# Kernel tuning notes

Measured on AMD Instinct MI355X. Metric: run time of the kernel, lower is better.

Reference implementation:

```python
import jax, jax.numpy as jnp
import numpy as np

B, S, D, H = 2, 2048, 1024, 16
DK = D // H


def setup_inputs() -> dict:
    key = jax.random.key(0)
    ks = jax.random.split(key, 12)
    s = 1.0 / np.sqrt(D)
    return {
        "query": jax.random.normal(ks[0], (B, S, D), dtype=jnp.float32),
        "key": jax.random.normal(ks[1], (B, S, D), dtype=jnp.float32),
        "value": jax.random.normal(ks[2], (B, S, D), dtype=jnp.float32),
        "mask": jax.random.randint(ks[3], (B, 1, 1, S), 0, 2, dtype=jnp.int32),
        "wq": jax.random.normal(ks[4], (D, D), dtype=jnp.float32) * s,
        "bq": jnp.zeros((D,), dtype=jnp.float32),
        "wk": jax.random.normal(ks[5], (D, D), dtype=jnp.float32) * s,
        "bk": jnp.zeros((D,), dtype=jnp.float32),
        "wv": jax.random.normal(ks[6], (D, D), dtype=jnp.float32) * s,
        "bv": jnp.zeros((D,), dtype=jnp.float32),
        "wo": jax.random.normal(ks[7], (D, D), dtype=jnp.float32) * s,
        "bo": jnp.zeros((D,), dtype=jnp.float32),
    }


def reference(query, key, value, mask, wq, bq, wk, bk, wv, bv, wo, bo):
    b, s, d = query.shape
    # torch Linear: y = x @ W^T + b, then split heads -> [B, H, S, dk]
    def proj(x, w, bias):
        return (x @ w.T + bias).reshape(b, -1, H, DK).transpose(0, 2, 1, 3)

    q = proj(query, wq, bq)
    k = proj(key, wk, bk)
    v = proj(value, wv, bv)

    scores = jnp.einsum("bhqd,bhkd->bhqk", q, k) / jnp.sqrt(jnp.float32(DK))
    scores = jnp.where(mask == 0, jnp.float32(-1e9), scores)
    attn = jax.nn.softmax(scores, axis=-1)  # [B,H,S,S]
    x = jnp.einsum("bhqk,bhkd->bhqd", attn, v)
    x = x.transpose(0, 2, 1, 3).reshape(b, s, d)
    return x @ wo.T + bo
```

## Files before the change

### kernel.cpp

```cpp
#include <hip/hip_runtime.h>
#include <math.h>

#define B_  2
#define S_  2048
#define D_  1024
#define H_  16
#define DK_ 64

typedef unsigned short u16;
typedef unsigned int u32;
typedef __bf16 bf16x8 __attribute__((ext_vector_type(8)));
typedef float f32x4 __attribute__((ext_vector_type(4)));
typedef float f32x16 __attribute__((ext_vector_type(16)));
typedef u32 u32x2 __attribute__((ext_vector_type(2)));
typedef u32 u32x4 __attribute__((ext_vector_type(4)));

typedef const __attribute__((address_space(1))) void* gas1_t;
typedef __attribute__((address_space(3))) void* las3_t;

__device__ __forceinline__ void gload_lds16(const void* g, void* l) {
    __builtin_amdgcn_global_load_lds((gas1_t)g, (las3_t)l, 16, 0, 0);
}

__device__ __forceinline__ u16 f2bf(float f) {
    union { float f; unsigned u; } v; v.f = f;
    return (u16)((v.u + 0x7fffu + ((v.u >> 16) & 1u)) >> 16);
}

__device__ __forceinline__ u32 pack_bf16_2(float lo, float hi) {
    union { float f; u32 u; } a, b;
    a.f = lo; b.f = hi;
    return __builtin_amdgcn_perm(b.u + 0x8000u, a.u + 0x8000u, 0x07060302u);
}

__device__ __forceinline__ u32 cvtpk_bf16(float lo, float hi) {
    u32 r;
    asm("v_cvt_pk_bf16_f32 %0, %1, %2" : "=v"(r) : "v"(lo), "v"(hi));
    return r;
}

__global__ __launch_bounds__(256)
void cast_all(const float* __restrict__ q, const float* __restrict__ k,
              const float* __restrict__ v, const float* __restrict__ wq,
              const float* __restrict__ wk, const float* __restrict__ wv,
              const float* __restrict__ wo, const int* __restrict__ mask,
              u16* __restrict__ qb, u16* __restrict__ kb, u16* __restrict__ vb,
              u16* __restrict__ wqb, u16* __restrict__ wkb, u16* __restrict__ wvb,
              u16* __restrict__ wob, float* __restrict__ mfac,
              float* __restrict__ nmaskf)
{
    const int bi = blockIdx.x;
    const int tid = threadIdx.x;
    if (bi >= 2064) {
        const int b = bi - 2064;
        __shared__ int red[256];
        int c = 0;
#pragma unroll
        for (int j = 0; j < 8; ++j)
            c += (mask[b * S_ + tid * 8 + j] == 0) ? 1 : 0;
        red[tid] = c;
        __syncthreads();
        for (int s = 128; s > 0; s >>= 1) {
            if (tid < s) red[tid] += red[tid + s];
            __syncthreads();
        }
        if (tid == 0) nmaskf[b] = (float)red[0];
        return;
    }
    if (bi >= 2048) {
        const int idx = (bi - 2048) * 256 + tid;
        mfac[idx] = mask[idx] ? 1.0f : 0.0f;
        return;
    }
#pragma unroll
    for (int j = 0; j < 8; ++j) {
        const int i = bi * 256 + tid + j * 524288;
        const float* src; u16* dst; int off;
        if (i < 3 * 1048576) {
            const int seg = i >> 20; off = i & 1048575;
            src = (seg == 0) ? q : (seg == 1) ? k : v;
            dst = (seg == 0) ? qb : (seg == 1) ? kb : vb;
        } else {
            const int jj = i - 3 * 1048576;
            const int seg = jj >> 18; off = jj & 262143;
            src = (seg == 0) ? wq : (seg == 1) ? wk : (seg == 2) ? wv : wo;
            dst = (seg == 0) ? wqb : (seg == 1) ? wkb : (seg == 2) ? wvb : wob;
        }
        const float4 val = ((const float4*)src)[off];
        uint2 o;
        o.x = pack_bf16_2(val.x, val.y);
        o.y = pack_bf16_2(val.z, val.w);
        ((uint2*)dst)[off] = o;
    }
}

template<int BM, int BN>
__device__ __forceinline__ void gemm_body(
    const u16* __restrict__ A, const u16* __restrict__ W,
    const float* __restrict__ bias, void* __restrict__ outp,
    float scale, int mode, int m0, int n0,
    const float* __restrict__ rowfac, const float* __restrict__ colfac)
{
    constexpr int MI = BM / 32;
    constexpr int NJ = BN / 32;
    __shared__ u16 sA[BM * 64];
    __shared__ u16 sW[BN * 64];

    const int tid  = threadIdx.x;
    const int wave = tid >> 6, lane = tid & 63;
    const int quad = lane >> 4, l16 = lane & 15;
    const int wm = (wave >> 1) * (BM / 2);
    const int wn = (wave & 1) * (BN / 2);
    const int srow = lane >> 3;
    const int scol = ((lane & 7) ^ srow) * 8;
    const int sw7  = l16 & 7;

    f32x4 acc[MI][NJ];
    const f32x4 zero = {0.f, 0.f, 0.f, 0.f};
#pragma unroll
    for (int i = 0; i < MI; ++i)
#pragma unroll
        for (int j = 0; j < NJ; ++j) acc[i][j] = zero;

    const u16* ast = A + (size_t)(m0 + wave * 8 + srow) * D_ + scol;
    const u16* wst = W + (size_t)(n0 + wave * 8 + srow) * D_ + scol;

    for (int k0 = 0; k0 < D_; k0 += 64) {
#pragma unroll
        for (int t = 0; t < BM / 32; ++t)
            gload_lds16(ast + (size_t)t * 32 * D_ + k0, sA + (wave + t * 4) * 512);
#pragma unroll
        for (int t = 0; t < BN / 32; ++t)
            gload_lds16(wst + (size_t)t * 32 * D_ + k0, sW + (wave + t * 4) * 512);
        __syncthreads();

#pragma unroll
        for (int kh = 0; kh < 2; ++kh) {
            const int phys = ((kh * 4 + quad) ^ sw7) * 8;
            bf16x8 af[MI], bfr[NJ];
#pragma unroll
            for (int i = 0; i < MI; ++i)
                af[i] = *(const bf16x8*)(sA + (wm + i * 16 + l16) * 64 + phys);
#pragma unroll
            for (int j = 0; j < NJ; ++j)
                bfr[j] = *(const bf16x8*)(sW + (wn + j * 16 + l16) * 64 + phys);
#pragma unroll
            for (int i = 0; i < MI; ++i)
#pragma unroll
                for (int j = 0; j < NJ; ++j)
                    acc[i][j] = __builtin_amdgcn_mfma_f32_16x16x32_bf16(af[i], bfr[j], acc[i][j], 0, 0, 0);
        }
        __syncthreads();
    }

#pragma unroll
    for (int i = 0; i < MI; ++i) {
        float rf4[4];
        if (mode == 1 && rowfac) {
#pragma unroll
            for (int r = 0; r < 4; ++r)
                rf4[r] = rowfac[m0 + wm + i * 16 + quad * 4 + r];
        }
#pragma unroll
        for (int j = 0; j < NJ; ++j) {
            const int n = n0 + wn + j * 16 + l16;
            if (mode == 3) {
                const float cf = colfac ? colfac[n] : 1.0f;
#pragma unroll
                for (int r = 0; r < 4; ++r) {
                    const int mp = m0 + wm + i * 16 + quad * 4 + r;
                    ((u16*)outp)[(size_t)mp * (B_ * S_) + n] = f2bf((acc[i][j][r] + bias[mp]) * cf);
                }
            } else {
                const float bn = bias[n];
#pragma unroll
                for (int r = 0; r < 4; ++r) {
                    const int m = m0 + wm + i * 16 + quad * 4 + r;
                    float v = acc[i][j][r] + bn;
                    if (mode == 0) {
                        ((float*)outp)[(size_t)m * D_ + n] = v;
                    } else {
                        v *= scale;
                        if (rowfac) v *= rf4[r];
                        const int b = m >> 11, s = m & (S_ - 1);
                        const int h = n >> 6, dk = n & 63;
                        ((u16*)outp)[(((size_t)(b * H_ + h)) * S_ + s) * DK_ + dk] = f2bf(v);
                    }
                }
            }
        }
    }
}

__global__ __launch_bounds__(256)
void qkv_gemm(const u16* __restrict__ qin, const u16* __restrict__ kin, const u16* __restrict__ vin,
              const u16* __restrict__ wqb, const u16* __restrict__ wkb, const u16* __restrict__ wvb,
              const float* __restrict__ bq, const float* __restrict__ bk, const float* __restrict__ bv,
              u16* __restrict__ Qp, u16* __restrict__ Kp, u16* __restrict__ Vt,
              const float* __restrict__ mfac)
{
    const int bid = blockIdx.x;
    const int swz = (bid & 7) * 192 + (bid >> 3);
    const int z   = swz >> 9;
    const int rem = swz & 511;

    if (z == 2) {
        const int mi = rem & 15, ni = rem >> 4;
        gemm_body<64, 128>(wvb, vin, bv, Vt, 1.0f, 3, mi * 64, ni * 128,
                           nullptr, mfac);
    } else {
        const int by = rem >> 3;
        const int bx = rem & 7;
        const u16* A = (z == 0) ? qin : kin;
        const u16* W = (z == 0) ? wqb : wkb;
        const float* bias = (z == 0) ? bq : bk;
        u16* outp = (z == 0) ? Qp : Kp;
        const float scale = (z == 0) ? 0.18033688011112042f : 1.0f;
        const float* rf = (z == 1) ? mfac : nullptr;
        gemm_body<64, 128>(A, W, bias, outp, scale, 1, by * 64, bx * 128,
                           rf, nullptr);
    }
}

__global__ __launch_bounds__(256)
void out_gemm(const u16* __restrict__ Xc, const u16* __restrict__ wob,
              const float* __restrict__ bo, float* __restrict__ out)
{
    const int bid = blockIdx.x;
    const int swz = (bid & 7) * 128 + (bid >> 3);
    const int by  = swz >> 4;
    const int bx  = swz & 15;
    gemm_body<64, 64>(Xc, wob, bo, out, 1.0f, 0, by * 64, bx * 64,
                      nullptr, nullptr);
}

__global__ __launch_bounds__(512, 4)
void attn_mfma(const u16* __restrict__ Qp, const u16* __restrict__ Kp,
               const u16* __restrict__ Vt, const float* __restrict__ nmaskf,
               u16* __restrict__ Xc)
{
    __shared__ u16 sKV[2][2][8192];

    const int tid  = threadIdx.x;
    const int wave = tid >> 6, lane = tid & 63;
    const int qg = wave & 3, kg = wave >> 2;
    const int l31 = lane & 31, hi = lane >> 5;
    const int bid = blockIdx.x;
    const int swz = (bid & 7) * 64 + (bid >> 3);
    const int qt = swz & 15;
    const int bh = swz >> 4;
    const int b  = bh >> 4;
    const int h  = bh & 15;
    const int lr  = lane >> 3;
    const int cl  = (lane & 7) ^ lr;
    const int sw5 = l31 & 7;

    const u16* Qb = Qp + ((size_t)bh * S_ + qt * 128) * DK_;
    const u16* Kb = Kp + (size_t)bh * S_ * DK_;
    const int vdk = (qg * 8 + lr) + 32 * (cl >> 2);
    const u16* Vsrc = Vt + (size_t)(h * 64 + vdk) * (B_ * S_) + b * S_ + (cl & 3) * 8;
    const u16* Ksrc = Kb + (size_t)(qg * 8 + lr) * DK_ + cl * 8;

    bf16x8 qf[4];
    {
        const u16* qrow = Qb + (size_t)(qg * 32 + l31) * DK_ + hi * 8;
        qf[0] = *(const bf16x8*)(qrow);
        qf[1] = *(const bf16x8*)(qrow + 16);
        qf[2] = *(const bf16x8*)(qrow + 32);
        qf[3] = *(const bf16x8*)(qrow + 48);
    }

    const u16* kpre = Ksrc + (size_t)kg * 64 * DK_;
    const u16* vpre = Vsrc + kg * 64;
    {
        u16* dst = sKV[kg][0];
        gload_lds16(kpre,                    dst + qg * 512);
        gload_lds16(kpre + (size_t)32 * DK_, dst + 2048 + qg * 512);
        gload_lds16(vpre,                    dst + 4096 + qg * 512);
        gload_lds16(vpre + 32,               dst + 6144 + qg * 512);
        kpre += (size_t)128 * DK_;
        vpre += 128;
    }

    f32x16 oc[2];
    const f32x16 z16 = {0.f,0.f,0.f,0.f,0.f,0.f,0.f,0.f,
                        0.f,0.f,0.f,0.f,0.f,0.f,0.f,0.f};
    oc[0] = z16; oc[1] = z16;
    float lsum = 0.f;

    for (int i = 0; i < 16; ++i) {
        __syncthreads();
        const int cur = i & 1;

        if (i < 15) {
            u16* dst = sKV[kg][cur ^ 1];
            gload_lds16(kpre,                    dst + qg * 512);
            gload_lds16(kpre + (size_t)32 * DK_, dst + 2048 + qg * 512);
            gload_lds16(vpre,                    dst + 4096 + qg * 512);
            gload_lds16(vpre + 32,               dst + 6144 + qg * 512);
            kpre += (size_t)128 * DK_;
            vpre += 128;
        }
        const u16* sKA = sKV[kg][cur];
        const u16* sKB = sKA + 2048;
        const u16* sVA = sKA + 4096;
        const u16* sVB = sKA + 6144;

        f32x16 sfrA, sfrB;
        {
            const bf16x8 a0 = *(const bf16x8*)(sKA + l31 * 64 + (((0 + hi) ^ sw5)) * 8);
            const bf16x8 a1 = *(const bf16x8*)(sKA + l31 * 64 + (((2 + hi) ^ sw5)) * 8);
            const bf16x8 a2 = *(const bf16x8*)(sKA + l31 * 64 + (((4 + hi) ^ sw5)) * 8);
            const bf16x8 a3 = *(const bf16x8*)(sKA + l31 * 64 + (((6 + hi) ^ sw5)) * 8);
            const bf16x8 b0 = *(const bf16x8*)(sKB + l31 * 64 + (((0 + hi) ^ sw5)) * 8);
            const bf16x8 b1 = *(const bf16x8*)(sKB + l31 * 64 + (((2 + hi) ^ sw5)) * 8);
            const bf16x8 b2 = *(const bf16x8*)(sKB + l31 * 64 + (((4 + hi) ^ sw5)) * 8);
            const bf16x8 b3 = *(const bf16x8*)(sKB + l31 * 64 + (((6 + hi) ^ sw5)) * 8);
            __builtin_amdgcn_s_setprio(1);
            sfrA = __builtin_amdgcn_mfma_f32_32x32x16_bf16(a0, qf[0], z16, 0, 0, 0);
            sfrB = __builtin_amdgcn_mfma_f32_32x32x16_bf16(b0, qf[0], z16, 0, 0, 0);
            sfrA = __builtin_amdgcn_mfma_f32_32x32x16_bf16(a1, qf[1], sfrA, 0, 0, 0);
            sfrB = __builtin_amdgcn_mfma_f32_32x32x16_bf16(b1, qf[1], sfrB, 0, 0, 0);
            sfrA = __builtin_amdgcn_mfma_f32_32x32x16_bf16(a2, qf[2], sfrA, 0, 0, 0);
            sfrB = __builtin_amdgcn_mfma_f32_32x32x16_bf16(b2, qf[2], sfrB, 0, 0, 0);
            sfrA = __builtin_amdgcn_mfma_f32_32x32x16_bf16(a3, qf[3], sfrA, 0, 0, 0);
            sfrB = __builtin_amdgcn_mfma_f32_32x32x16_bf16(b3, qf[3], sfrB, 0, 0, 0);
            __builtin_amdgcn_s_setprio(0);
        }

        {
            float p[16];
#pragma unroll
            for (int r = 0; r < 16; ++r) p[r] = __builtin_amdgcn_exp2f(sfrA[r]);
            const float s0 = (p[0] + p[1]) + (p[2] + p[3]);
            const float s1 = (p[4] + p[5]) + (p[6] + p[7]);
            const float s2 = (p[8] + p[9]) + (p[10] + p[11]);
            const float s3 = (p[12] + p[13]) + (p[14] + p[15]);
            lsum += (s0 + s1) + (s2 + s3);
            const u32 W00 = cvtpk_bf16(p[0], p[1]);
            const u32 W01 = cvtpk_bf16(p[2], p[3]);
            const u32 W10 = cvtpk_bf16(p[4], p[5]);
            const u32 W11 = cvtpk_bf16(p[6], p[7]);
            const u32 W20 = cvtpk_bf16(p[8], p[9]);
            const u32 W21 = cvtpk_bf16(p[10], p[11]);
            const u32 W30 = cvtpk_bf16(p[12], p[13]);
            const u32 W31 = cvtpk_bf16(p[14], p[15]);
            const u32x2 e0 = __builtin_amdgcn_permlane32_swap(W00, W10, false, false);
            const u32x2 e1 = __builtin_amdgcn_permlane32_swap(W01, W11, false, false);
            const u32x2 e2 = __builtin_amdgcn_permlane32_swap(W20, W30, false, false);
            const u32x2 e3 = __builtin_amdgcn_permlane32_swap(W21, W31, false, false);
            u32x4 A0 = { e0[0], e1[0], e0[1], e1[1] };
            u32x4 A1 = { e2[0], e3[0], e2[1], e3[1] };
            const bf16x8 pa0 = *(const bf16x8*)&A0;
            const bf16x8 pa1 = *(const bf16x8*)&A1;
            const bf16x8 v00 = *(const bf16x8*)(sVA + l31 * 64 + (((0 + hi) ^ sw5)) * 8);
            const bf16x8 v01 = *(const bf16x8*)(sVA + l31 * 64 + (((2 + hi) ^ sw5)) * 8);
            const bf16x8 v10 = *(const bf16x8*)(sVA + l31 * 64 + (((4 + hi) ^ sw5)) * 8);
            const bf16x8 v11 = *(const bf16x8*)(sVA + l31 * 64 + (((6 + hi) ^ sw5)) * 8);
            __builtin_amdgcn_s_setprio(1);
            oc[0] = __builtin_amdgcn_mfma_f32_32x32x16_bf16(pa0, v00, oc[0], 0, 0, 0);
            oc[1] = __builtin_amdgcn_mfma_f32_32x32x16_bf16(pa0, v10, oc[1], 0, 0, 0);
            oc[0] = __builtin_amdgcn_mfma_f32_32x32x16_bf16(pa1, v01, oc[0], 0, 0, 0);
            oc[1] = __builtin_amdgcn_mfma_f32_32x32x16_bf16(pa1, v11, oc[1], 0, 0, 0);
            __builtin_amdgcn_s_setprio(0);
        }

        {
            float p[16];
#pragma unroll
            for (int r = 0; r < 16; ++r) p[r] = __builtin_amdgcn_exp2f(sfrB[r]);
            const float s0 = (p[0] + p[1]) + (p[2] + p[3]);
            const float s1 = (p[4] + p[5]) + (p[6] + p[7]);
            const float s2 = (p[8] + p[9]) + (p[10] + p[11]);
            const float s3 = (p[12] + p[13]) + (p[14] + p[15]);
            lsum += (s0 + s1) + (s2 + s3);
            const u32 W00 = cvtpk_bf16(p[0], p[1]);
            const u32 W01 = cvtpk_bf16(p[2], p[3]);
            const u32 W10 = cvtpk_bf16(p[4], p[5]);
            const u32 W11 = cvtpk_bf16(p[6], p[7]);
            const u32 W20 = cvtpk_bf16(p[8], p[9]);
            const u32 W21 = cvtpk_bf16(p[10], p[11]);
            const u32 W30 = cvtpk_bf16(p[12], p[13]);
            const u32 W31 = cvtpk_bf16(p[14], p[15]);
            const u32x2 e0 = __builtin_amdgcn_permlane32_swap(W00, W10, false, false);
            const u32x2 e1 = __builtin_amdgcn_permlane32_swap(W01, W11, false, false);
            const u32x2 e2 = __builtin_amdgcn_permlane32_swap(W20, W30, false, false);
            const u32x2 e3 = __builtin_amdgcn_permlane32_swap(W21, W31, false, false);
            u32x4 A0 = { e0[0], e1[0], e0[1], e1[1] };
            u32x4 A1 = { e2[0], e3[0], e2[1], e3[1] };
            const bf16x8 pa0 = *(const bf16x8*)&A0;
            const bf16x8 pa1 = *(const bf16x8*)&A1;
            const bf16x8 v00 = *(const bf16x8*)(sVB + l31 * 64 + (((0 + hi) ^ sw5)) * 8);
            const bf16x8 v01 = *(const bf16x8*)(sVB + l31 * 64 + (((2 + hi) ^ sw5)) * 8);
            const bf16x8 v10 = *(const bf16x8*)(sVB + l31 * 64 + (((4 + hi) ^ sw5)) * 8);
            const bf16x8 v11 = *(const bf16x8*)(sVB + l31 * 64 + (((6 + hi) ^ sw5)) * 8);
            __builtin_amdgcn_s_setprio(1);
            oc[0] = __builtin_amdgcn_mfma_f32_32x32x16_bf16(pa0, v00, oc[0], 0, 0, 0);
            oc[1] = __builtin_amdgcn_mfma_f32_32x32x16_bf16(pa0, v10, oc[1], 0, 0, 0);
            oc[0] = __builtin_amdgcn_mfma_f32_32x32x16_bf16(pa1, v01, oc[0], 0, 0, 0);
            oc[1] = __builtin_amdgcn_mfma_f32_32x32x16_bf16(pa1, v11, oc[1], 0, 0, 0);
            __builtin_amdgcn_s_setprio(0);
        }
    }

    {
        union { float f; u32 u; } lu; lu.f = lsum;
        const u32x2 lr2 = __builtin_amdgcn_permlane32_swap(lu.u, lu.u, false, false);
        union { u32 u; float f; } pu; pu.u = hi ? lr2[0] : lr2[1];
        lsum += pu.f;
    }

    __syncthreads();
    float* sO = (float*)&sKV[0][0][0];
    float* sL = (float*)((char*)sO + 32768);
    if (hi == 0) sL[kg * 128 + qg * 32 + l31] = lsum;
    if (kg == 1) {
#pragma unroll
        for (int dh = 0; dh < 2; ++dh)
#pragma unroll
            for (int g = 0; g < 4; ++g) {
                f32x4 t = { oc[dh][g * 4 + 0], oc[dh][g * 4 + 1],
                            oc[dh][g * 4 + 2], oc[dh][g * 4 + 3] };
                *(f32x4*)(sO + qg * 2048 + ((dh * 4 + g) * 2 + hi) * 128 + l31 * 4) = t;
            }
    }
    __syncthreads();
    if (kg == 0) {
        const float nm = nmaskf[b];
#pragma unroll
        for (int g = 0; g < 4; ++g) {
            const f32x4 oA = *(const f32x4*)(sO + qg * 2048 + ((0 + g) * 2 + hi) * 128 + l31 * 4);
            const f32x4 oB = *(const f32x4*)(sO + qg * 2048 + ((4 + g) * 2 + hi) * 128 + l31 * 4);
#pragma unroll
            for (int rr = 0; rr < 4; ++rr) {
                const int qrow = rr + 8 * g + 4 * hi;
                const float inv = __builtin_amdgcn_rcpf(
                    sL[qg * 32 + qrow] + sL[128 + qg * 32 + qrow] - nm);
                const int s = qt * 128 + qg * 32 + qrow;
                const size_t base = ((size_t)(b * S_ + s)) * D_ + h * 64 + l31;
                Xc[base]      = f2bf((oc[0][g * 4 + rr] + oA[rr]) * inv);
                Xc[base + 32] = f2bf((oc[1][g * 4 + rr] + oB[rr]) * inv);
            }
        }
    }
}

extern "C" void kernel_launch(void* const* d_in, const int* in_sizes, int n_in,
                              void* d_out, int out_size, void* d_ws, size_t ws_size,
                              hipStream_t stream)
{
    (void)in_sizes; (void)n_in; (void)out_size; (void)ws_size;

    const float* query = (const float*)d_in[0];
    const float* key   = (const float*)d_in[1];
    const float* value = (const float*)d_in[2];
    const int*   mask  = (const int*)d_in[3];
    const float* wq    = (const float*)d_in[4];
    const float* bq    = (const float*)d_in[5];
    const float* wk    = (const float*)d_in[6];
    const float* bk    = (const float*)d_in[7];
    const float* wv    = (const float*)d_in[8];
    const float* bv    = (const float*)d_in[9];
    const float* wo    = (const float*)d_in[10];
    const float* bo    = (const float*)d_in[11];

    const size_t NE = (size_t)B_ * S_ * D_;
    const size_t WE = (size_t)D_ * D_;

    u16* qb  = (u16*)d_ws;
    u16* kb  = qb + NE;
    u16* vb  = kb + NE;
    u16* wqb = vb + NE;
    u16* wkb = wqb + WE;
    u16* wvb = wkb + WE;
    u16* wob = wvb + WE;
    u16* Qp  = wob + WE;
    u16* Kp  = Qp + NE;
    u16* Vt  = Kp + NE;
    float* mfac   = (float*)(Vt + NE);
    float* nmaskf = mfac + 4096;
    u16* Xc  = qb;

    cast_all<<<2066, 256, 0, stream>>>(query, key, value, wq, wk, wv, wo, mask,
                                       qb, kb, vb, wqb, wkb, wvb, wob, mfac, nmaskf);

    qkv_gemm<<<1536, 256, 0, stream>>>(
        qb, kb, vb, wqb, wkb, wvb, bq, bk, bv, Qp, Kp, Vt, mfac);

    attn_mfma<<<512, 512, 0, stream>>>(Qp, Kp, Vt, nmaskf, Xc);

    out_gemm<<<1024, 256, 0, stream>>>(Xc, wob, bo, (float*)d_out);
}
```

Baseline: 211.1 us.

## Split attention block into 64-query tiles with four-way key split

The attention kernel now gives each block 64 query rows instead of 128, and its 8 waves are arranged as 2 query groups by 4 key groups instead of 4 by 2. Each wave handles one 32-key slab per iteration instead of two, and the grid doubles to 1024 blocks. The final reduction merges three partial outputs and four row sums through shared memory. The aim is more blocks in flight and shorter per-wave dependency chains, at the cost of reloading K/V per query tile, a heavier cross-wave reduction, and less independent MFMA work per wave to hide latency.

```diff
diff --git a/kernel.cpp b/kernel.cpp
--- a/kernel.cpp
+++ b/kernel.cpp
@@ -239,23 +239,23 @@
                const u16* __restrict__ Vt, const float* __restrict__ nmaskf,
                u16* __restrict__ Xc)
 {
-    __shared__ u16 sKV[2][2][8192];
+    __shared__ u16 sKV[4][2][4096];
 
     const int tid  = threadIdx.x;
     const int wave = tid >> 6, lane = tid & 63;
-    const int qg = wave & 3, kg = wave >> 2;
+    const int qg = wave & 1, kg = wave >> 1;
     const int l31 = lane & 31, hi = lane >> 5;
     const int bid = blockIdx.x;
-    const int swz = (bid & 7) * 64 + (bid >> 3);
-    const int qt = swz & 15;
-    const int bh = swz >> 4;
+    const int swz = (bid & 7) * 128 + (bid >> 3);
+    const int qt = swz & 31;
+    const int bh = swz >> 5;
     const int b  = bh >> 4;
     const int h  = bh & 15;
     const int lr  = lane >> 3;
     const int cl  = (lane & 7) ^ lr;
     const int sw5 = l31 & 7;
 
-    const u16* Qb = Qp + ((size_t)bh * S_ + qt * 128) * DK_;
+    const u16* Qb = Qp + ((size_t)bh * S_ + qt * 64) * DK_;
     const u16* Kb = Kp + (size_t)bh * S_ * DK_;
     const int vdk = (qg * 8 + lr) + 32 * (cl >> 2);
     const u16* Vsrc = Vt + (size_t)(h * 64 + vdk) * (B_ * S_) + b * S_ + (cl & 3) * 8;
@@ -270,14 +270,14 @@
         qf[3] = *(const bf16x8*)(qrow + 48);
     }
 
-    const u16* kpre = Ksrc + (size_t)kg * 64 * DK_;
-    const u16* vpre = Vsrc + kg * 64;
+    const u16* kpre = Ksrc + (size_t)kg * 32 * DK_;
+    const u16* vpre = Vsrc + kg * 32;
     {
-        u16* dst = sKV[kg][0];
-        gload_lds16(kpre,                    dst + qg * 512);
-        gload_lds16(kpre + (size_t)32 * DK_, dst + 2048 + qg * 512);
-        gload_lds16(vpre,                    dst + 4096 + qg * 512);
-        gload_lds16(vpre + 32,               dst + 6144 + qg * 512);
+        u16* dst = &sKV[kg][0][0];
+        gload_lds16(kpre,                            dst + qg * 512);
+        gload_lds16(kpre + (size_t)16 * DK_,         dst + (qg + 2) * 512);
+        gload_lds16(vpre,                            dst + 2048 + qg * 512);
+        gload_lds16(vpre + (size_t)16 * (B_ * S_),   dst + 2048 + (qg + 2) * 512);
         kpre += (size_t)128 * DK_;
         vpre += 128;
     }
@@ -293,70 +293,63 @@
         const int cur = i & 1;
 
         if (i < 15) {
-            u16* dst = sKV[kg][cur ^ 1];
-            gload_lds16(kpre,                    dst + qg * 512);
-            gload_lds16(kpre + (size_t)32 * DK_, dst + 2048 + qg * 512);
-            gload_lds16(vpre,                    dst + 4096 + qg * 512);
-            gload_lds16(vpre + 32,               dst + 6144 + qg * 512);
+            u16* dst = &sKV[kg][cur ^ 1][0];
+            gload_lds16(kpre,                            dst + qg * 512);
+            gload_lds16(kpre + (size_t)16 * DK_,         dst + (qg + 2) * 512);
+            gload_lds16(vpre,                            dst + 2048 + qg * 512);
+            gload_lds16(vpre + (size_t)16 * (B_ * S_),   dst + 2048 + (qg + 2) * 512);
             kpre += (size_t)128 * DK_;
             vpre += 128;
         }
-        const u16* sKA = sKV[kg][cur];
-        const u16* sKB = sKA + 2048;
-        const u16* sVA = sKA + 4096;
-        const u16* sVB = sKA + 6144;
-
-        f32x16 sfrA, sfrB;
+        const u16* sK = &sKV[kg][cur][0];
+        const u16* sV = sK + 2048;
+
+        f32x16 sfr;
         {
-            const bf16x8 a0 = *(const bf16x8*)(sKA + l31 * 64 + (((0 + hi) ^ sw5)) * 8);
-            const bf16x8 a1 = *(const bf16x8*)(sKA + l31 * 64 + (((2 + hi) ^ sw5)) * 8);
-            const bf16x8 a2 = *(const bf16x8*)(sKA + l31 * 64 + (((4 + hi) ^ sw5)) * 8);
-            const bf16x8 a3 = *(const bf16x8*)(sKA + l31 * 64 + (((6 + hi) ^ sw5)) * 8);
-            const bf16x8 b0 = *(const bf16x8*)(sKB + l31 * 64 + (((0 + hi) ^ sw5)) * 8);
-            const bf16x8 b1 = *(const bf16x8*)(sKB + l31 * 64 + (((2 + hi) ^ sw5)) * 8);
-            const bf16x8 b2 = *(const bf16x8*)(sKB + l31 * 64 + (((4 + hi) ^ sw5)) * 8);
-            const bf16x8 b3 = *(const bf16x8*)(sKB + l31 * 64 + (((6 + hi) ^ sw5)) * 8);
+            const bf16x8 k0 = *(const bf16x8*)(sK + l31 * 64 + (((0 + hi) ^ sw5)) * 8);
+            const bf16x8 k1 = *(const bf16x8*)(sK + l31 * 64 + (((2 + hi) ^ sw5)) * 8);
+            const bf16x8 k2 = *(const bf16x8*)(sK + l31 * 64 + (((4 + hi) ^ sw5)) * 8);
+            const bf16x8 k3 = *(const bf16x8*)(sK + l31 * 64 + (((6 + hi) ^ sw5)) * 8);
             __builtin_amdgcn_s_setprio(1);
-            sfrA = __builtin_amdgcn_mfma_f32_32x32x16_bf16(a0, qf[0], z16, 0, 0, 0);
-            sfrB = __builtin_amdgcn_mfma_f32_32x32x16_bf16(b0, qf[0], z16, 0, 0, 0);
-            sfrA = __builtin_amdgcn_mfma_f32_32x32x16_bf16(a1, qf[1], sfrA, 0, 0, 0);
-            sfrB = __builtin_amdgcn_mfma_f32_32x32x16_bf16(b1, qf[1], sfrB, 0, 0, 0);
-            sfrA = __builtin_amdgcn_mfma_f32_32x32x16_bf16(a2, qf[2], sfrA, 0, 0, 0);
-            sfrB = __builtin_amdgcn_mfma_f32_32x32x16_bf16(b2, qf[2], sfrB, 0, 0, 0);
-            sfrA = __builtin_amdgcn_mfma_f32_32x32x16_bf16(a3, qf[3], sfrA, 0, 0, 0);
-            sfrB = __builtin_amdgcn_mfma_f32_32x32x16_bf16(b3, qf[3], sfrB, 0, 0, 0);
+            sfr = __builtin_amdgcn_mfma_f32_32x32x16_bf16(k0, qf[0], z16, 0, 0, 0);
+            sfr = __builtin_amdgcn_mfma_f32_32x32x16_bf16(k1, qf[1], sfr, 0, 0, 0);
+            sfr = __builtin_amdgcn_mfma_f32_32x32x16_bf16(k2, qf[2], sfr, 0, 0, 0);
+            sfr = __builtin_amdgcn_mfma_f32_32x32x16_bf16(k3, qf[3], sfr, 0, 0, 0);
             __builtin_amdgcn_s_setprio(0);
         }
 
+        float p[16];
+#pragma unroll
+        for (int r = 0; r < 16; ++r) p[r] = __builtin_amdgcn_exp2f(sfr[r]);
         {
-            float p[16];
-#pragma unroll
-            for (int r = 0; r < 16; ++r) p[r] = __builtin_amdgcn_exp2f(sfrA[r]);
             const float s0 = (p[0] + p[1]) + (p[2] + p[3]);
             const float s1 = (p[4] + p[5]) + (p[6] + p[7]);
             const float s2 = (p[8] + p[9]) + (p[10] + p[11]);
             const float s3 = (p[12] + p[13]) + (p[14] + p[15]);
             lsum += (s0 + s1) + (s2 + s3);
-            const u32 W00 = cvtpk_bf16(p[0], p[1]);
-            const u32 W01 = cvtpk_bf16(p[2], p[3]);
-            const u32 W10 = cvtpk_bf16(p[4], p[5]);
-            const u32 W11 = cvtpk_bf16(p[6], p[7]);
-            const u32 W20 = cvtpk_bf16(p[8], p[9]);
-            const u32 W21 = cvtpk_bf16(p[10], p[11]);
-            const u32 W30 = cvtpk_bf16(p[12], p[13]);
-            const u32 W31 = cvtpk_bf16(p[14], p[15]);
-            const u32x2 e0 = __builtin_amdgcn_permlane32_swap(W00, W10, false, false);
-            const u32x2 e1 = __builtin_amdgcn_permlane32_swap(W01, W11, false, false);
-            const u32x2 e2 = __builtin_amdgcn_permlane32_swap(W20, W30, false, false);
-            const u32x2 e3 = __builtin_amdgcn_permlane32_swap(W21, W31, false, false);
-            u32x4 A0 = { e0[0], e1[0], e0[1], e1[1] };
-            u32x4 A1 = { e2[0], e3[0], e2[1], e3[1] };
-            const bf16x8 pa0 = *(const bf16x8*)&A0;
-            const bf16x8 pa1 = *(const bf16x8*)&A1;
-            const bf16x8 v00 = *(const bf16x8*)(sVA + l31 * 64 + (((0 + hi) ^ sw5)) * 8);
-            const bf16x8 v01 = *(const bf16x8*)(sVA + l31 * 64 + (((2 + hi) ^ sw5)) * 8);
-            const bf16x8 v10 = *(const bf16x8*)(sVA + l31 * 64 + (((4 + hi) ^ sw5)) * 8);
-            const bf16x8 v11 = *(const bf16x8*)(sVA + l31 * 64 + (((6 + hi) ^ sw5)) * 8);
+        }
+        const u32 W00 = cvtpk_bf16(p[0], p[1]);
+        const u32 W01 = cvtpk_bf16(p[2], p[3]);
+        const u32 W10 = cvtpk_bf16(p[4], p[5]);
+        const u32 W11 = cvtpk_bf16(p[6], p[7]);
+        const u32 W20 = cvtpk_bf16(p[8], p[9]);
+        const u32 W21 = cvtpk_bf16(p[10], p[11]);
+        const u32 W30 = cvtpk_bf16(p[12], p[13]);
+        const u32 W31 = cvtpk_bf16(p[14], p[15]);
+        const u32x2 e0 = __builtin_amdgcn_permlane32_swap(W00, W10, false, false);
+        const u32x2 e1 = __builtin_amdgcn_permlane32_swap(W01, W11, false, false);
+        const u32x2 e2 = __builtin_amdgcn_permlane32_swap(W20, W30, false, false);
+        const u32x2 e3 = __builtin_amdgcn_permlane32_swap(W21, W31, false, false);
+        u32x4 A0 = { e0[0], e1[0], e0[1], e1[1] };
+        u32x4 A1 = { e2[0], e3[0], e2[1], e3[1] };
+        const bf16x8 pa0 = *(const bf16x8*)&A0;
+        const bf16x8 pa1 = *(const bf16x8*)&A1;
+
+        {
+            const bf16x8 v00 = *(const bf16x8*)(sV + l31 * 64 + (((0 + hi) ^ sw5)) * 8);
+            const bf16x8 v01 = *(const bf16x8*)(sV + l31 * 64 + (((2 + hi) ^ sw5)) * 8);
+            const bf16x8 v10 = *(const bf16x8*)(sV + l31 * 64 + (((4 + hi) ^ sw5)) * 8);
+            const bf16x8 v11 = *(const bf16x8*)(sV + l31 * 64 + (((6 + hi) ^ sw5)) * 8);
             __builtin_amdgcn_s_setprio(1);
             oc[0] = __builtin_amdgcn_mfma_f32_32x32x16_bf16(pa0, v00, oc[0], 0, 0, 0);
             oc[1] = __builtin_amdgcn_mfma_f32_32x32x16_bf16(pa0, v10, oc[1], 0, 0, 0);
@@ -364,43 +357,6 @@
             oc[1] = __builtin_amdgcn_mfma_f32_32x32x16_bf16(pa1, v11, oc[1], 0, 0, 0);
             __builtin_amdgcn_s_setprio(0);
         }
-
-        {
-            float p[16];
-#pragma unroll
-            for (int r = 0; r < 16; ++r) p[r] = __builtin_amdgcn_exp2f(sfrB[r]);
-            const float s0 = (p[0] + p[1]) + (p[2] + p[3]);
-            const float s1 = (p[4] + p[5]) + (p[6] + p[7]);
-            const float s2 = (p[8] + p[9]) + (p[10] + p[11]);
-            const float s3 = (p[12] + p[13]) + (p[14] + p[15]);
-            lsum += (s0 + s1) + (s2 + s3);
-            const u32 W00 = cvtpk_bf16(p[0], p[1]);
-            const u32 W01 = cvtpk_bf16(p[2], p[3]);
-            const u32 W10 = cvtpk_bf16(p[4], p[5]);
-            const u32 W11 = cvtpk_bf16(p[6], p[7]);
-            const u32 W20 = cvtpk_bf16(p[8], p[9]);
-            const u32 W21 = cvtpk_bf16(p[10], p[11]);
-            const u32 W30 = cvtpk_bf16(p[12], p[13]);
-            const u32 W31 = cvtpk_bf16(p[14], p[15]);
-            const u32x2 e0 = __builtin_amdgcn_permlane32_swap(W00, W10, false, false);
-            const u32x2 e1 = __builtin_amdgcn_permlane32_swap(W01, W11, false, false);
-            const u32x2 e2 = __builtin_amdgcn_permlane32_swap(W20, W30, false, false);
-            const u32x2 e3 = __builtin_amdgcn_permlane32_swap(W21, W31, false, false);
-            u32x4 A0 = { e0[0], e1[0], e0[1], e1[1] };
-            u32x4 A1 = { e2[0], e3[0], e2[1], e3[1] };
-            const bf16x8 pa0 = *(const bf16x8*)&A0;
-            const bf16x8 pa1 = *(const bf16x8*)&A1;
-            const bf16x8 v00 = *(const bf16x8*)(sVB + l31 * 64 + (((0 + hi) ^ sw5)) * 8);
-            const bf16x8 v01 = *(const bf16x8*)(sVB + l31 * 64 + (((2 + hi) ^ sw5)) * 8);
-            const bf16x8 v10 = *(const bf16x8*)(sVB + l31 * 64 + (((4 + hi) ^ sw5)) * 8);
-            const bf16x8 v11 = *(const bf16x8*)(sVB + l31 * 64 + (((6 + hi) ^ sw5)) * 8);
-            __builtin_amdgcn_s_setprio(1);
-            oc[0] = __builtin_amdgcn_mfma_f32_32x32x16_bf16(pa0, v00, oc[0], 0, 0, 0);
-            oc[1] = __builtin_amdgcn_mfma_f32_32x32x16_bf16(pa0, v10, oc[1], 0, 0, 0);
-            oc[0] = __builtin_amdgcn_mfma_f32_32x32x16_bf16(pa1, v01, oc[0], 0, 0, 0);
-            oc[1] = __builtin_amdgcn_mfma_f32_32x32x16_bf16(pa1, v11, oc[1], 0, 0, 0);
-            __builtin_amdgcn_s_setprio(0);
-        }
     }
 
     {
@@ -412,16 +368,17 @@
 
     __syncthreads();
     float* sO = (float*)&sKV[0][0][0];
-    float* sL = (float*)((char*)sO + 32768);
-    if (hi == 0) sL[kg * 128 + qg * 32 + l31] = lsum;
-    if (kg == 1) {
+    float* sL = (float*)((char*)&sKV[0][0][0] + 49152);
+    if (hi == 0) sL[kg * 64 + qg * 32 + l31] = lsum;
+    if (kg != 0) {
+        const int slot = (kg - 1) * 2 + qg;
 #pragma unroll
         for (int dh = 0; dh < 2; ++dh)
 #pragma unroll
             for (int g = 0; g < 4; ++g) {
                 f32x4 t = { oc[dh][g * 4 + 0], oc[dh][g * 4 + 1],
                             oc[dh][g * 4 + 2], oc[dh][g * 4 + 3] };
-                *(f32x4*)(sO + qg * 2048 + ((dh * 4 + g) * 2 + hi) * 128 + l31 * 4) = t;
+                *(f32x4*)(sO + slot * 2048 + ((dh * 4 + g) * 2 + hi) * 128 + l31 * 4) = t;
             }
     }
     __syncthreads();
@@ -429,17 +386,23 @@
         const float nm = nmaskf[b];
 #pragma unroll
         for (int g = 0; g < 4; ++g) {
-            const f32x4 oA = *(const f32x4*)(sO + qg * 2048 + ((0 + g) * 2 + hi) * 128 + l31 * 4);
-            const f32x4 oB = *(const f32x4*)(sO + qg * 2048 + ((4 + g) * 2 + hi) * 128 + l31 * 4);
+            f32x4 a0, b0, c0, a1, b1, c1;
+            a0 = *(const f32x4*)(sO + (0 + qg) * 2048 + ((0 + g) * 2 + hi) * 128 + l31 * 4);
+            b0 = *(const f32x4*)(sO + (2 + qg) * 2048 + ((0 + g) * 2 + hi) * 128 + l31 * 4);
+            c0 = *(const f32x4*)(sO + (4 + qg) * 2048 + ((0 + g) * 2 + hi) * 128 + l31 * 4);
+            a1 = *(const f32x4*)(sO + (0 + qg) * 2048 + ((4 + g) * 2 + hi) * 128 + l31 * 4);
+            b1 = *(const f32x4*)(sO + (2 + qg) * 2048 + ((4 + g) * 2 + hi) * 128 + l31 * 4);
+            c1 = *(const f32x4*)(sO + (4 + qg) * 2048 + ((4 + g) * 2 + hi) * 128 + l31 * 4);
 #pragma unroll
             for (int rr = 0; rr < 4; ++rr) {
                 const int qrow = rr + 8 * g + 4 * hi;
                 const float inv = __builtin_amdgcn_rcpf(
-                    sL[qg * 32 + qrow] + sL[128 + qg * 32 + qrow] - nm);
-                const int s = qt * 128 + qg * 32 + qrow;
+                    sL[qg * 32 + qrow] + sL[64 + qg * 32 + qrow] +
+                    sL[128 + qg * 32 + qrow] + sL[192 + qg * 32 + qrow] - nm);
+                const int s = qt * 64 + qg * 32 + qrow;
                 const size_t base = ((size_t)(b * S_ + s)) * D_ + h * 64 + l31;
-                Xc[base]      = f2bf((oc[0][g * 4 + rr] + oA[rr]) * inv);
-                Xc[base + 32] = f2bf((oc[1][g * 4 + rr] + oB[rr]) * inv);
+                Xc[base]      = f2bf((oc[0][g * 4 + rr] + a0[rr] + b0[rr] + c0[rr]) * inv);
+                Xc[base + 32] = f2bf((oc[1][g * 4 + rr] + a1[rr] + b1[rr] + c1[rr]) * inv);
             }
         }
     }
@@ -487,7 +450,7 @@
     qkv_gemm<<<1536, 256, 0, stream>>>(
         qb, kb, vb, wqb, wkb, wvb, bq, bk, bv, Qp, Kp, Vt, mfac);
 
-    attn_mfma<<<512, 512, 0, stream>>>(Qp, Kp, Vt, nmaskf, Xc);
+    attn_mfma<<<1024, 512, 0, stream>>>(Qp, Kp, Vt, nmaskf, Xc);
 
     out_gemm<<<1024, 256, 0, stream>>>(Xc, wob, bo, (float*)d_out);
 }
```

After: 219.4 us. +3.9%, slower.

## Fuse activation fp32-to-bf16 cast into QKV GEMM tile loads

Applied to the files above, without the earlier changes.

Drops the separate cast pass over the query, key and value activations and has the QKV GEMM read fp32 inputs directly, converting them to bf16 in registers before writing to LDS. The cast kernel now handles only weights and mask. This removes a full write and re-read of three bf16 activation tensors. In exchange, the activation tiles are re-read as fp32 (twice the bytes) by every N-tile block, and the loads go through registers instead of async direct-to-LDS loads, which can add latency and register pressure.

```diff
diff --git a/kernel.cpp b/kernel.cpp
--- a/kernel.cpp
+++ b/kernel.cpp
@@ -40,19 +40,17 @@
 }
 
 __global__ __launch_bounds__(256)
-void cast_all(const float* __restrict__ q, const float* __restrict__ k,
-              const float* __restrict__ v, const float* __restrict__ wq,
-              const float* __restrict__ wk, const float* __restrict__ wv,
-              const float* __restrict__ wo, const int* __restrict__ mask,
-              u16* __restrict__ qb, u16* __restrict__ kb, u16* __restrict__ vb,
-              u16* __restrict__ wqb, u16* __restrict__ wkb, u16* __restrict__ wvb,
-              u16* __restrict__ wob, float* __restrict__ mfac,
-              float* __restrict__ nmaskf)
+void cast_all(const float* __restrict__ wq, const float* __restrict__ wk,
+              const float* __restrict__ wv, const float* __restrict__ wo,
+              const int* __restrict__ mask,
+              u16* __restrict__ wqb, u16* __restrict__ wkb,
+              u16* __restrict__ wvb, u16* __restrict__ wob,
+              float* __restrict__ mfac, float* __restrict__ nmaskf)
 {
     const int bi = blockIdx.x;
     const int tid = threadIdx.x;
-    if (bi >= 2064) {
-        const int b = bi - 2064;
+    if (bi >= 528) {
+        const int b = bi - 528;
         __shared__ int red[256];
         int c = 0;
 #pragma unroll
@@ -67,25 +65,18 @@
         if (tid == 0) nmaskf[b] = (float)red[0];
         return;
     }
-    if (bi >= 2048) {
-        const int idx = (bi - 2048) * 256 + tid;
+    if (bi >= 512) {
+        const int idx = (bi - 512) * 256 + tid;
         mfac[idx] = mask[idx] ? 1.0f : 0.0f;
         return;
     }
 #pragma unroll
     for (int j = 0; j < 8; ++j) {
-        const int i = bi * 256 + tid + j * 524288;
-        const float* src; u16* dst; int off;
-        if (i < 3 * 1048576) {
-            const int seg = i >> 20; off = i & 1048575;
-            src = (seg == 0) ? q : (seg == 1) ? k : v;
-            dst = (seg == 0) ? qb : (seg == 1) ? kb : vb;
-        } else {
-            const int jj = i - 3 * 1048576;
-            const int seg = jj >> 18; off = jj & 262143;
-            src = (seg == 0) ? wq : (seg == 1) ? wk : (seg == 2) ? wv : wo;
-            dst = (seg == 0) ? wqb : (seg == 1) ? wkb : (seg == 2) ? wvb : wob;
-        }
+        const int i = bi * 256 + tid + j * 131072;
+        const int seg = i >> 18;
+        const int off = i & 262143;
+        const float* src = (seg == 0) ? wq : (seg == 1) ? wk : (seg == 2) ? wv : wo;
+        u16* dst = (seg == 0) ? wqb : (seg == 1) ? wkb : (seg == 2) ? wvb : wob;
         const float4 val = ((const float4*)src)[off];
         uint2 o;
         o.x = pack_bf16_2(val.x, val.y);
@@ -94,9 +85,9 @@
     }
 }
 
-template<int BM, int BN>
+template<int BM, int BN, bool AF32, bool WF32>
 __device__ __forceinline__ void gemm_body(
-    const u16* __restrict__ A, const u16* __restrict__ W,
+    const void* __restrict__ A, const void* __restrict__ W,
     const float* __restrict__ bias, void* __restrict__ outp,
     float scale, int mode, int m0, int n0,
     const float* __restrict__ rowfac, const float* __restrict__ colfac)
@@ -122,16 +113,44 @@
 #pragma unroll
         for (int j = 0; j < NJ; ++j) acc[i][j] = zero;
 
-    const u16* ast = A + (size_t)(m0 + wave * 8 + srow) * D_ + scol;
-    const u16* wst = W + (size_t)(n0 + wave * 8 + srow) * D_ + scol;
+    const size_t aoff = (size_t)(m0 + wave * 8 + srow) * D_ + scol;
+    const size_t woff = (size_t)(n0 + wave * 8 + srow) * D_ + scol;
+    const u16*   astB = (const u16*)A + aoff;
+    const float* astF = (const float*)A + aoff;
+    const u16*   wstB = (const u16*)W + woff;
+    const float* wstF = (const float*)W + woff;
 
     for (int k0 = 0; k0 < D_; k0 += 64) {
-#pragma unroll
-        for (int t = 0; t < BM / 32; ++t)
-            gload_lds16(ast + (size_t)t * 32 * D_ + k0, sA + (wave + t * 4) * 512);
-#pragma unroll
-        for (int t = 0; t < BN / 32; ++t)
-            gload_lds16(wst + (size_t)t * 32 * D_ + k0, sW + (wave + t * 4) * 512);
+        if constexpr (AF32) {
+#pragma unroll
+            for (int t = 0; t < BM / 32; ++t) {
+                const float* src = astF + (size_t)t * 32 * D_ + k0;
+                const float4 v0 = *(const float4*)(src);
+                const float4 v1 = *(const float4*)(src + 4);
+                u32x4 w = { cvtpk_bf16(v0.x, v0.y), cvtpk_bf16(v0.z, v0.w),
+                            cvtpk_bf16(v1.x, v1.y), cvtpk_bf16(v1.z, v1.w) };
+                *(u32x4*)(sA + (wave + t * 4) * 512 + lane * 8) = w;
+            }
+        } else {
+#pragma unroll
+            for (int t = 0; t < BM / 32; ++t)
+                gload_lds16(astB + (size_t)t * 32 * D_ + k0, sA + (wave + t * 4) * 512);
+        }
+        if constexpr (WF32) {
+#pragma unroll
+            for (int t = 0; t < BN / 32; ++t) {
+                const float* src = wstF + (size_t)t * 32 * D_ + k0;
+                const float4 v0 = *(const float4*)(src);
+                const float4 v1 = *(const float4*)(src + 4);
+                u32x4 w = { cvtpk_bf16(v0.x, v0.y), cvtpk_bf16(v0.z, v0.w),
+                            cvtpk_bf16(v1.x, v1.y), cvtpk_bf16(v1.z, v1.w) };
+                *(u32x4*)(sW + (wave + t * 4) * 512 + lane * 8) = w;
+            }
+        } else {
+#pragma unroll
+            for (int t = 0; t < BN / 32; ++t)
+                gload_lds16(wstB + (size_t)t * 32 * D_ + k0, sW + (wave + t * 4) * 512);
+        }
         __syncthreads();
 
 #pragma unroll
@@ -193,7 +212,8 @@
 }
 
 __global__ __launch_bounds__(256)
-void qkv_gemm(const u16* __restrict__ qin, const u16* __restrict__ kin, const u16* __restrict__ vin,
+void qkv_gemm(const float* __restrict__ qF, const float* __restrict__ kF,
+              const float* __restrict__ vF,
               const u16* __restrict__ wqb, const u16* __restrict__ wkb, const u16* __restrict__ wvb,
               const float* __restrict__ bq, const float* __restrict__ bk, const float* __restrict__ bv,
               u16* __restrict__ Qp, u16* __restrict__ Kp, u16* __restrict__ Vt,
@@ -206,19 +226,19 @@
 
     if (z == 2) {
         const int mi = rem & 15, ni = rem >> 4;
-        gemm_body<64, 128>(wvb, vin, bv, Vt, 1.0f, 3, mi * 64, ni * 128,
-                           nullptr, mfac);
+        gemm_body<64, 128, false, true>(wvb, vF, bv, Vt, 1.0f, 3, mi * 64, ni * 128,
+                                        nullptr, mfac);
     } else {
         const int by = rem >> 3;
         const int bx = rem & 7;
-        const u16* A = (z == 0) ? qin : kin;
+        const void* A = (z == 0) ? (const void*)qF : (const void*)kF;
         const u16* W = (z == 0) ? wqb : wkb;
         const float* bias = (z == 0) ? bq : bk;
         u16* outp = (z == 0) ? Qp : Kp;
         const float scale = (z == 0) ? 0.18033688011112042f : 1.0f;
         const float* rf = (z == 1) ? mfac : nullptr;
-        gemm_body<64, 128>(A, W, bias, outp, scale, 1, by * 64, bx * 128,
-                           rf, nullptr);
+        gemm_body<64, 128, true, false>(A, W, bias, outp, scale, 1, by * 64, bx * 128,
+                                        rf, nullptr);
     }
 }
 
@@ -230,8 +250,8 @@
     const int swz = (bid & 7) * 128 + (bid >> 3);
     const int by  = swz >> 4;
     const int bx  = swz & 15;
-    gemm_body<64, 64>(Xc, wob, bo, out, 1.0f, 0, by * 64, bx * 64,
-                      nullptr, nullptr);
+    gemm_body<64, 64, false, false>(Xc, wob, bo, out, 1.0f, 0, by * 64, bx * 64,
+                                    nullptr, nullptr);
 }
 
 __global__ __launch_bounds__(512, 4)
@@ -481,11 +501,11 @@
     float* nmaskf = mfac + 4096;
     u16* Xc  = qb;
 
-    cast_all<<<2066, 256, 0, stream>>>(query, key, value, wq, wk, wv, wo, mask,
-                                       qb, kb, vb, wqb, wkb, wvb, wob, mfac, nmaskf);
+    cast_all<<<530, 256, 0, stream>>>(wq, wk, wv, wo, mask,
+                                      wqb, wkb, wvb, wob, mfac, nmaskf);
 
     qkv_gemm<<<1536, 256, 0, stream>>>(
-        qb, kb, vb, wqb, wkb, wvb, bq, bk, bv, Qp, Kp, Vt, mfac);
+        query, key, value, wqb, wkb, wvb, bq, bk, bv, Qp, Kp, Vt, mfac);
 
     attn_mfma<<<512, 512, 0, stream>>>(Qp, Kp, Vt, nmaskf, Xc);
 
```

New measurement: 220.2 us. +4.3%, slower.
